# Kernel tuning notes

Hardware: AMD Instinct MI355X
Metric: run time of the kernel (lower is better)

The kernel has to match this reference:

```python
import jax, jax.numpy as jnp
import numpy as np

B, T, C, H = 65536, 100, 7, 2  # batch, timesteps, covariates, lstm hidden


def setup_inputs() -> dict:
    key = jax.random.key(0)
    ks = iter(jax.random.split(key, 32))
    def rn(shape, s=0.1):
        return jax.random.normal(next(ks), shape, dtype=jnp.float32) * s
    inp = {"x": jax.random.normal(next(ks), (B, T, C), dtype=jnp.float32)}
    for l, din in ((0, C), (1, 2 * H)):
        for suf in ("", "r"):
            inp[f"w_ih_l{l}{suf}"] = rn((4 * H, din))
            inp[f"w_hh_l{l}{suf}"] = rn((4 * H, H))
            inp[f"b_ih_l{l}{suf}"] = rn((4 * H,))
            inp[f"b_hh_l{l}{suf}"] = rn((4 * H,))
    inp["fc1_w"] = rn((64, 4 * T))
    inp["fc1_b"] = rn((64,))
    inp["fc2_w"] = rn((20, 64))
    inp["fc2_b"] = rn((20,))
    return inp


def _lstm_dir(xw, w_hh, b_hh, reverse):
    # xw: [T, B, 4H] precomputed input projection (x @ W_ih.T + b_ih)
    if reverse:
        xw = xw[::-1]
    h0 = jnp.zeros((xw.shape[1], H), xw.dtype)
    c0 = jnp.zeros((xw.shape[1], H), xw.dtype)

    def step(carry, gx):
        h, c = carry
        g = gx + h @ w_hh.T + b_hh            # [B, 4H]
        i, f, gg, o = jnp.split(g, 4, axis=-1)  # torch gate order i,f,g,o
        c = jax.nn.sigmoid(f) * c + jax.nn.sigmoid(i) * jnp.tanh(gg)
        h = jax.nn.sigmoid(o) * jnp.tanh(c)
        return (h, c), h

    _, hs = jax.lax.scan(step, (h0, c0), xw)
    if reverse:
        hs = hs[::-1]
    return hs  # [T, B, H]


def _bilstm_layer(x_tbf, w_ih_f, w_hh_f, b_ih_f, b_hh_f,
                  w_ih_b, w_hh_b, b_ih_b, b_hh_b):
    xw_f = jnp.einsum('tbc,gc->tbg', x_tbf, w_ih_f) + b_ih_f
    xw_b = jnp.einsum('tbc,gc->tbg', x_tbf, w_ih_b) + b_ih_b
    hf = _lstm_dir(xw_f, w_hh_f, b_hh_f, False)
    hb = _lstm_dir(xw_b, w_hh_b, b_hh_b, True)
    return jnp.concatenate([hf, hb], axis=-1)  # [T, B, 2H]


def reference(x,
              w_ih_l0, w_hh_l0, b_ih_l0, b_hh_l0,
              w_ih_l0r, w_hh_l0r, b_ih_l0r, b_hh_l0r,
              w_ih_l1, w_hh_l1, b_ih_l1, b_hh_l1,
              w_ih_l1r, w_hh_l1r, b_ih_l1r, b_hh_l1r,
              fc1_w, fc1_b, fc2_w, fc2_b):
    xt = jnp.transpose(x.reshape(-1, T, C), (1, 0, 2))  # [T, B, C] time-major
    h1 = _bilstm_layer(xt, w_ih_l0, w_hh_l0, b_ih_l0, b_hh_l0,
                       w_ih_l0r, w_hh_l0r, b_ih_l0r, b_hh_l0r)
    h2 = _bilstm_layer(h1, w_ih_l1, w_hh_l1, b_ih_l1, b_hh_l1,
                       w_ih_l1r, w_hh_l1r, b_ih_l1r, b_hh_l1r)
    out = jnp.transpose(h2, (1, 0, 2)).reshape(-1, 4 * T)  # flatten [B, 4T]
    out = jax.nn.relu(out)                  # relu BEFORE fc1, as in original
    out = jax.nn.relu(out @ fc1_w.T + fc1_b)
    return out @ fc2_w.T + fc2_b            # [B, 20]
```

## Files before the change

kernel.cpp:

```cpp
#include <hip/hip_runtime.h>

#define Bn 65536
#define Tn 100
#define Cn 7

__device__ __forceinline__ float fast_rcp(float x) { return __builtin_amdgcn_rcpf(x); }
__device__ __forceinline__ float sig_f(float x) { return fast_rcp(1.f + __expf(-x)); }
__device__ __forceinline__ float tanh_f(float x) { return 1.f - 2.f * fast_rcp(__expf(2.f * x) + 1.f); }
__device__ __forceinline__ float rdlane(float v, int l) {
    return __int_as_float(__builtin_amdgcn_readlane(__float_as_int(v), l));
}

typedef const __attribute__((address_space(1))) void* gp_t;
typedef __attribute__((address_space(3))) void* sp_t;
__device__ __forceinline__ void async_copy_dw(const float* g, float* l) {
    __builtin_amdgcn_global_load_lds((gp_t)g, (sp_t)l, 4, 0, 0);
}

__global__ void fc1t_kernel(const float* __restrict__ fc1_w, float* __restrict__ fc1_wt) {
    int idx = blockIdx.x * 256 + threadIdx.x;
    if (idx < 400 * 64) {
        int col = idx >> 6;
        int k = idx & 63;
        fc1_wt[idx] = fc1_w[k * 400 + col];
    }
}

__global__ __launch_bounds__(256) void l0_kernel(
    const float* __restrict__ x,
    const float* __restrict__ wih_f, const float* __restrict__ whh_f,
    const float* __restrict__ bih_f, const float* __restrict__ bhh_f,
    const float* __restrict__ wih_r, const float* __restrict__ whh_r,
    const float* __restrict__ bih_r, const float* __restrict__ bhh_r,
    float2* __restrict__ h1f2)
{
    __shared__ float xs[2][2][4480];

    const int tid  = threadIdx.x;
    const int rev  = tid >> 7;
    const int s    = tid & 127;
    const int b    = blockIdx.x * 128 + s;
    const int w    = tid >> 6;
    const int lane = tid & 63;
    const int sdir = w >> 1;
    const int half = w & 1;

    const float* wih = rev ? wih_r : wih_f;
    const float* whh = rev ? whh_r : whh_f;
    const float* bih = rev ? bih_r : bih_f;
    const float* bhh = rev ? bhh_r : bhh_f;

    float wi[56], wh[16], bias[8];
#pragma unroll
    for (int k = 0; k < 56; ++k) wi[k] = wih[k];
#pragma unroll
    for (int k = 0; k < 16; ++k) wh[k] = whh[k];
#pragma unroll
    for (int k = 0; k < 8; ++k) bias[k] = bih[k] + bhh[k];

    const int e  = (lane >= 35) ? 1 : 0;
    const int r0 = lane - 35 * e;
    const int s0 = half * 64 + e;
    const float* xsamp = x + (size_t)(blockIdx.x * 128 + s0) * 700;

    auto stage = [&](int ch, int p) {
        const int off = sdir ? (665 - 35 * ch) : (35 * ch);
        const float* g = xsamp + off + r0;
        float* l = &xs[p][sdir][half * 2240 + lane];
        int r = r0;
#pragma unroll
        for (int i = 0; i < 35; ++i) {
            async_copy_dw(g, l);
            l += 64;
            const int c = (r >= 6) ? 1 : 0;
            g += c ? 1394 : 729;
            r += c ? -6 : 29;
        }
    };

    float h0 = 0.f, h1v = 0.f, c0 = 0.f, c1 = 0.f;

    stage(0, 0);
#pragma unroll 1
    for (int ch = 0; ch < 20; ++ch) {
        __builtin_amdgcn_s_waitcnt(0);
        __syncthreads();
        if (ch < 19) stage(ch + 1, (ch + 1) & 1);

        const int t0 = rev ? (95 - 5 * ch) : (5 * ch);
        const float* xbuf = &xs[ch & 1][rev][0];
#pragma unroll 1
        for (int tt = 0; tt < 5; ++tt) {
            const int rr = rev ? (4 - tt) : tt;
            const int t  = t0 + rr;
            const float* xrow = xbuf + s * 35 + rr * 7;

            float g[8];
#pragma unroll
            for (int k = 0; k < 8; ++k) g[k] = bias[k];
#pragma unroll
            for (int c = 0; c < 7; ++c) {
                const float xv = xrow[c];
#pragma unroll
                for (int k = 0; k < 8; ++k) g[k] = fmaf(wi[k * 7 + c], xv, g[k]);
            }
#pragma unroll
            for (int k = 0; k < 8; ++k)
                g[k] = fmaf(wh[k * 2], h0, fmaf(wh[k * 2 + 1], h1v, g[k]));

            const float i0 = sig_f(g[0]), i1 = sig_f(g[1]);
            const float f0 = sig_f(g[2]), f1 = sig_f(g[3]);
            const float q0 = tanh_f(g[4]), q1 = tanh_f(g[5]);
            const float o0 = sig_f(g[6]), o1 = sig_f(g[7]);
            c0 = fmaf(f0, c0, i0 * q0);
            c1 = fmaf(f1, c1, i1 * q1);
            h0  = o0 * tanh_f(c0);
            h1v = o1 * tanh_f(c1);

            h1f2[((size_t)t * 2 + rev) * Bn + b] = make_float2(h0, h1v);
        }
    }
}

__global__ __launch_bounds__(256) void l1fc_kernel(
    const float2* __restrict__ hin,
    const float* __restrict__ wih_f, const float* __restrict__ whh_f,
    const float* __restrict__ bih_f, const float* __restrict__ bhh_f,
    const float* __restrict__ wih_r, const float* __restrict__ whh_r,
    const float* __restrict__ bih_r, const float* __restrict__ bhh_r,
    const float* __restrict__ fc1_wt,
    const float* __restrict__ fc1_b,
    const float* __restrict__ fc2_w,
    const float* __restrict__ fc2_b,
    float* __restrict__ out)
{
    __shared__ float ebuf[128 * 65];

    const int tid  = threadIdx.x;
    const int w    = tid >> 6;
    const int lane = tid & 63;
    const int d    = w >> 1;
    const int half = w & 1;
    const int sm   = half * 64 + lane;
    const size_t b = (size_t)blockIdx.x * 128 + sm;

    const float* wih = d ? wih_r : wih_f;
    const float* whh = d ? whh_r : whh_f;
    const float* bih = d ? bih_r : bih_f;
    const float* bhh = d ? bhh_r : bhh_f;

    float wi[32], wh[16], bias[8];
#pragma unroll
    for (int k = 0; k < 32; ++k) wi[k] = wih[k];
#pragma unroll
    for (int k = 0; k < 16; ++k) wh[k] = whh[k];
#pragma unroll
    for (int k = 0; k < 8; ++k) bias[k] = bih[k] + bhh[k];

    const float b1 = fc1_b[lane];

    float acc[64];
#pragma unroll
    for (int k = 0; k < 64; ++k) acc[k] = 0.f;

    auto tstep = [&](int st) { return d ? 99 - st : st; };
    auto hload = [&](int t, float2& uF, float2& uR) {
        uF = hin[((size_t)t * 2) * Bn + b];
        uR = hin[((size_t)t * 2 + 1) * Bn + b];
    };
    auto wrow = [&](int t) { return fc1_wt + ((size_t)t * 4 + 2 * d) * 64 + lane; };

    float2 aF, aR, p1F, p1R, p2F, p2R;
    hload(tstep(0), aF, aR);
    hload(tstep(1), p1F, p1R);
    hload(tstep(2), p2F, p2R);
    float wt0, wt1;
    { const float* wr = wrow(tstep(0)); wt0 = wr[0]; wt1 = wr[64]; }

    float h0 = 0.f, h1v = 0.f, c0 = 0.f, c1 = 0.f;

#pragma unroll 1
    for (int st = 0; st < 100; ++st) {
        const int sp = (st + 3 <= 99) ? st + 3 : 99;
        float2 nF, nR;
        hload(tstep(sp), nF, nR);
        const float* wr = wrow(tstep((st + 1 <= 99) ? st + 1 : 99));
        const float nw0 = wr[0], nw1 = wr[64];

        float g[8];
#pragma unroll
        for (int k = 0; k < 8; ++k) {
            g[k] = bias[k];
            g[k] = fmaf(wi[k * 4 + 0], aF.x, g[k]);
            g[k] = fmaf(wi[k * 4 + 1], aF.y, g[k]);
            g[k] = fmaf(wi[k * 4 + 2], aR.x, g[k]);
            g[k] = fmaf(wi[k * 4 + 3], aR.y, g[k]);
            g[k] = fmaf(wh[k * 2], h0, fmaf(wh[k * 2 + 1], h1v, g[k]));
        }
        const float i0 = sig_f(g[0]), i1 = sig_f(g[1]);
        const float f0 = sig_f(g[2]), f1 = sig_f(g[3]);
        const float q0 = tanh_f(g[4]), q1 = tanh_f(g[5]);
        const float o0 = sig_f(g[6]), o1 = sig_f(g[7]);
        c0 = fmaf(f0, c0, i0 * q0);
        c1 = fmaf(f1, c1, i1 * q1);
        h0  = o0 * tanh_f(c0);
        h1v = o1 * tanh_f(c1);

        const float v0 = fmaxf(h0, 0.f);
        const float v1 = fmaxf(h1v, 0.f);
#pragma unroll
        for (int j = 0; j < 64; ++j)
            acc[j] = fmaf(wt0, rdlane(v0, j), fmaf(wt1, rdlane(v1, j), acc[j]));

        aF = p1F; aR = p1R; p1F = p2F; p1R = p2R; p2F = nF; p2R = nR;
        wt0 = nw0; wt1 = nw1;
    }

    if (d) {
#pragma unroll
        for (int j = 0; j < 64; ++j) ebuf[(half * 64 + j) * 65 + lane] = acc[j];
    }
    __syncthreads();
    if (!d) {
#pragma unroll
        for (int j = 0; j < 64; ++j) {
            const int row = half * 64 + j;
            const float z = acc[j] + ebuf[row * 65 + lane] + b1;
            ebuf[row * 65 + lane] = fmaxf(z, 0.f);
        }
    }
    __syncthreads();

    const int sm2 = tid & 127;
    const int og  = (tid >> 7) * 10;
    float z[64];
#pragma unroll
    for (int k = 0; k < 64; ++k) z[k] = ebuf[sm2 * 65 + k];
    float y[10];
#pragma unroll
    for (int o = 0; o < 10; ++o) {
        float r2 = fc2_b[og + o];
#pragma unroll
        for (int k = 0; k < 64; ++k) r2 = fmaf(fc2_w[(og + o) * 64 + k], z[k], r2);
        y[o] = r2;
    }
    __syncthreads();
#pragma unroll
    for (int o = 0; o < 10; ++o) ebuf[sm2 * 20 + og + o] = y[o];
    __syncthreads();
    for (int f = tid; f < 2560; f += 256)
        out[(size_t)blockIdx.x * 2560 + f] = ebuf[f];
}

extern "C" void kernel_launch(void* const* d_in, const int* in_sizes, int n_in,
                              void* d_out, int out_size, void* d_ws, size_t ws_size,
                              hipStream_t stream) {
    const float* x = (const float*)d_in[0];
    const float* w_ih_l0  = (const float*)d_in[1];
    const float* w_hh_l0  = (const float*)d_in[2];
    const float* b_ih_l0  = (const float*)d_in[3];
    const float* b_hh_l0  = (const float*)d_in[4];
    const float* w_ih_l0r = (const float*)d_in[5];
    const float* w_hh_l0r = (const float*)d_in[6];
    const float* b_ih_l0r = (const float*)d_in[7];
    const float* b_hh_l0r = (const float*)d_in[8];
    const float* w_ih_l1  = (const float*)d_in[9];
    const float* w_hh_l1  = (const float*)d_in[10];
    const float* b_ih_l1  = (const float*)d_in[11];
    const float* b_hh_l1  = (const float*)d_in[12];
    const float* w_ih_l1r = (const float*)d_in[13];
    const float* w_hh_l1r = (const float*)d_in[14];
    const float* b_ih_l1r = (const float*)d_in[15];
    const float* b_hh_l1r = (const float*)d_in[16];
    const float* fc1_w = (const float*)d_in[17];
    const float* fc1_b = (const float*)d_in[18];
    const float* fc2_w = (const float*)d_in[19];
    const float* fc2_b = (const float*)d_in[20];

    float2* h1f2  = (float2*)d_ws;
    float* fc1_wt = (float*)((char*)d_ws + (size_t)Tn * 4 * Bn * sizeof(float));

    fc1t_kernel<<<100, 256, 0, stream>>>(fc1_w, fc1_wt);
    l0_kernel<<<512, 256, 0, stream>>>(x,
        w_ih_l0, w_hh_l0, b_ih_l0, b_hh_l0,
        w_ih_l0r, w_hh_l0r, b_ih_l0r, b_hh_l0r, h1f2);
    l1fc_kernel<<<512, 256, 0, stream>>>(h1f2,
        w_ih_l1, w_hh_l1, b_ih_l1, b_hh_l1,
        w_ih_l1r, w_hh_l1r, b_ih_l1r, b_hh_l1r,
        fc1_wt, fc1_b, fc2_w, fc2_b, (float*)d_out);
}
```

Before: 490.4 us.

## Compute fc1 with bf16 MFMA over staged LSTM outputs instead of readlane FMAs

Replaces the per-timestep 64-wide readlane/FMA accumulation of fc1 with staging relu'd layer-1 hidden states as packed bf16 in LDS, in chunks of 25 timesteps. Each chunk then runs 16x16x32 bf16 MFMA tiles against a pre-arranged bf16 copy of fc1 weights built by a new prep kernel. This removes the large scalar-broadcast FMA loop from the recurrence and frees the 64-float accumulator registers. In exchange it adds per-chunk block syncs and LDS traffic, and the bf16 rounding of activations and weights lowers precision.

```diff
diff --git a/kernel.cpp b/kernel.cpp
--- a/kernel.cpp
+++ b/kernel.cpp
@@ -4,11 +4,15 @@
 #define Tn 100
 #define Cn 7
 
+typedef short short8 __attribute__((ext_vector_type(8)));
+typedef float float4v __attribute__((ext_vector_type(4)));
+
 __device__ __forceinline__ float fast_rcp(float x) { return __builtin_amdgcn_rcpf(x); }
 __device__ __forceinline__ float sig_f(float x) { return fast_rcp(1.f + __expf(-x)); }
 __device__ __forceinline__ float tanh_f(float x) { return 1.f - 2.f * fast_rcp(__expf(2.f * x) + 1.f); }
-__device__ __forceinline__ float rdlane(float v, int l) {
-    return __int_as_float(__builtin_amdgcn_readlane(__float_as_int(v), l));
+__device__ __forceinline__ unsigned bf16rne(float x) {
+    unsigned u = __float_as_uint(x);
+    return (u + 0x7fffu + ((u >> 16) & 1u)) >> 16;
 }
 
 typedef const __attribute__((address_space(1))) void* gp_t;
@@ -17,13 +21,13 @@
     __builtin_amdgcn_global_load_lds((gp_t)g, (sp_t)l, 4, 0, 0);
 }
 
-__global__ void fc1t_kernel(const float* __restrict__ fc1_w, float* __restrict__ fc1_wt) {
+__global__ void w2prep_kernel(const float* __restrict__ fc1_w, unsigned short* __restrict__ w2g) {
     int idx = blockIdx.x * 256 + threadIdx.x;
-    if (idx < 400 * 64) {
-        int col = idx >> 6;
-        int k = idx & 63;
-        fc1_wt[idx] = fc1_w[k * 400 + col];
-    }
+    int w = idx >> 13, d = (idx >> 12) & 1, n = (idx >> 6) & 63, kk = idx & 63;
+    int tt = kk >> 1, i = kk & 1;
+    int t = d ? (99 - 25 * w - tt) : (25 * w + tt);
+    float v = (kk < 50) ? fc1_w[n * 400 + 4 * t + 2 * d + i] : 0.f;
+    w2g[idx] = (unsigned short)bf16rne(v);
 }
 
 __global__ __launch_bounds__(256) void l0_kernel(
@@ -128,19 +132,20 @@
     const float* __restrict__ bih_f, const float* __restrict__ bhh_f,
     const float* __restrict__ wih_r, const float* __restrict__ whh_r,
     const float* __restrict__ bih_r, const float* __restrict__ bhh_r,
-    const float* __restrict__ fc1_wt,
+    const float4* __restrict__ w2g,
     const float* __restrict__ fc1_b,
     const float* __restrict__ fc2_w,
     const float* __restrict__ fc2_b,
     float* __restrict__ out)
 {
-    __shared__ float ebuf[128 * 65];
+    __shared__ unsigned a2[2 * 128 * 36];
+    __shared__ unsigned w2[2 * 64 * 36];
 
     const int tid  = threadIdx.x;
-    const int w    = tid >> 6;
+    const int ww   = tid >> 6;
     const int lane = tid & 63;
-    const int d    = w >> 1;
-    const int half = w & 1;
+    const int d    = ww >> 1;
+    const int half = ww & 1;
     const int sm   = half * 64 + lane;
     const size_t b = (size_t)blockIdx.x * 128 + sm;
 
@@ -157,85 +162,124 @@
 #pragma unroll
     for (int k = 0; k < 8; ++k) bias[k] = bih[k] + bhh[k];
 
-    const float b1 = fc1_b[lane];
-
-    float acc[64];
-#pragma unroll
-    for (int k = 0; k < 64; ++k) acc[k] = 0.f;
+    float4v acc[2][4];
+#pragma unroll
+    for (int mt = 0; mt < 2; ++mt)
+#pragma unroll
+        for (int nt = 0; nt < 4; ++nt) acc[mt][nt] = (float4v){0.f, 0.f, 0.f, 0.f};
+
+    for (int i2 = tid; i2 < 2 * 128 * 36; i2 += 256) a2[i2] = 0u;
+    __syncthreads();
 
     auto tstep = [&](int st) { return d ? 99 - st : st; };
     auto hload = [&](int t, float2& uF, float2& uR) {
         uF = hin[((size_t)t * 2) * Bn + b];
         uR = hin[((size_t)t * 2 + 1) * Bn + b];
     };
-    auto wrow = [&](int t) { return fc1_wt + ((size_t)t * 4 + 2 * d) * 64 + lane; };
 
     float2 aF, aR, p1F, p1R, p2F, p2R;
     hload(tstep(0), aF, aR);
     hload(tstep(1), p1F, p1R);
     hload(tstep(2), p2F, p2R);
-    float wt0, wt1;
-    { const float* wr = wrow(tstep(0)); wt0 = wr[0]; wt1 = wr[64]; }
 
     float h0 = 0.f, h1v = 0.f, c0 = 0.f, c1 = 0.f;
+    const int cbase = tid * 4;
 
 #pragma unroll 1
-    for (int st = 0; st < 100; ++st) {
-        const int sp = (st + 3 <= 99) ? st + 3 : 99;
-        float2 nF, nR;
-        hload(tstep(sp), nF, nR);
-        const float* wr = wrow(tstep((st + 1 <= 99) ? st + 1 : 99));
-        const float nw0 = wr[0], nw1 = wr[64];
-
-        float g[8];
-#pragma unroll
-        for (int k = 0; k < 8; ++k) {
-            g[k] = bias[k];
-            g[k] = fmaf(wi[k * 4 + 0], aF.x, g[k]);
-            g[k] = fmaf(wi[k * 4 + 1], aF.y, g[k]);
-            g[k] = fmaf(wi[k * 4 + 2], aR.x, g[k]);
-            g[k] = fmaf(wi[k * 4 + 3], aR.y, g[k]);
-            g[k] = fmaf(wh[k * 2], h0, fmaf(wh[k * 2 + 1], h1v, g[k]));
-        }
-        const float i0 = sig_f(g[0]), i1 = sig_f(g[1]);
-        const float f0 = sig_f(g[2]), f1 = sig_f(g[3]);
-        const float q0 = tanh_f(g[4]), q1 = tanh_f(g[5]);
-        const float o0 = sig_f(g[6]), o1 = sig_f(g[7]);
-        c0 = fmaf(f0, c0, i0 * q0);
-        c1 = fmaf(f1, c1, i1 * q1);
-        h0  = o0 * tanh_f(c0);
-        h1v = o1 * tanh_f(c1);
-
-        const float v0 = fmaxf(h0, 0.f);
-        const float v1 = fmaxf(h1v, 0.f);
-#pragma unroll
-        for (int j = 0; j < 64; ++j)
-            acc[j] = fmaf(wt0, rdlane(v0, j), fmaf(wt1, rdlane(v1, j), acc[j]));
-
-        aF = p1F; aR = p1R; p1F = p2F; p1R = p2R; p2F = nF; p2R = nR;
-        wt0 = nw0; wt1 = nw1;
+    for (int w = 0; w < 4; ++w) {
+        float4 wl[4];
+#pragma unroll
+        for (int j = 0; j < 4; ++j) wl[j] = w2g[w * 1024 + cbase + j];
+
+#pragma unroll 1
+        for (int tt = 0; tt < 25; ++tt) {
+            const int st = 25 * w + tt;
+            const int sp = (st + 3 <= 99) ? st + 3 : 99;
+            float2 nF, nR;
+            hload(tstep(sp), nF, nR);
+
+            float g[8];
+#pragma unroll
+            for (int k = 0; k < 8; ++k) {
+                g[k] = bias[k];
+                g[k] = fmaf(wi[k * 4 + 0], aF.x, g[k]);
+                g[k] = fmaf(wi[k * 4 + 1], aF.y, g[k]);
+                g[k] = fmaf(wi[k * 4 + 2], aR.x, g[k]);
+                g[k] = fmaf(wi[k * 4 + 3], aR.y, g[k]);
+                g[k] = fmaf(wh[k * 2], h0, fmaf(wh[k * 2 + 1], h1v, g[k]));
+            }
+            const float i0 = sig_f(g[0]), i1 = sig_f(g[1]);
+            const float f0 = sig_f(g[2]), f1 = sig_f(g[3]);
+            const float q0 = tanh_f(g[4]), q1 = tanh_f(g[5]);
+            const float o0 = sig_f(g[6]), o1 = sig_f(g[7]);
+            c0 = fmaf(f0, c0, i0 * q0);
+            c1 = fmaf(f1, c1, i1 * q1);
+            h0  = o0 * tanh_f(c0);
+            h1v = o1 * tanh_f(c1);
+
+            const unsigned vpk = bf16rne(fmaxf(h0, 0.f)) | (bf16rne(fmaxf(h1v, 0.f)) << 16);
+            a2[d * 4608 + sm * 36 + tt] = vpk;
+
+            aF = p1F; aR = p1R; p1F = p2F; p1R = p2R; p2F = nF; p2R = nR;
+        }
+
+#pragma unroll
+        for (int j = 0; j < 4; ++j) {
+            const int c = cbase + j;
+            const int dst = (((c >> 9) << 6) + ((c >> 3) & 63)) * 36 + (c & 7) * 4;
+            *(float4*)(&w2[dst]) = wl[j];
+        }
+        __syncthreads();
+
+        {
+            const int q = lane >> 4, l16 = lane & 15;
+#pragma unroll
+            for (int dd = 0; dd < 2; ++dd) {
+#pragma unroll
+                for (int kt = 0; kt < 2; ++kt) {
+                    short8 av[2], bv[4];
+#pragma unroll
+                    for (int mt = 0; mt < 2; ++mt) {
+                        const int srow = ww * 32 + mt * 16 + l16;
+                        av[mt] = *(const short8*)&a2[dd * 4608 + srow * 36 + kt * 16 + q * 4];
+                    }
+#pragma unroll
+                    for (int nt = 0; nt < 4; ++nt)
+                        bv[nt] = *(const short8*)&w2[(dd * 64 + nt * 16 + l16) * 36 + kt * 16 + q * 4];
+#pragma unroll
+                    for (int mt = 0; mt < 2; ++mt)
+#pragma unroll
+                        for (int nt = 0; nt < 4; ++nt)
+                            acc[mt][nt] = __builtin_amdgcn_mfma_f32_16x16x32_bf16(
+                                av[mt], bv[nt], acc[mt][nt], 0, 0, 0);
+                }
+            }
+        }
+        __syncthreads();
     }
 
-    if (d) {
-#pragma unroll
-        for (int j = 0; j < 64; ++j) ebuf[(half * 64 + j) * 65 + lane] = acc[j];
+    {
+        const int q = lane >> 4, l16 = lane & 15;
+        float* eb = (float*)a2;
+#pragma unroll
+        for (int mt = 0; mt < 2; ++mt)
+#pragma unroll
+            for (int nt = 0; nt < 4; ++nt)
+#pragma unroll
+                for (int r = 0; r < 4; ++r) {
+                    const int sl = ww * 32 + mt * 16 + q * 4 + r;
+                    const int cl = nt * 16 + l16;
+                    eb[sl * 65 + cl] = acc[mt][nt][r];
+                }
     }
     __syncthreads();
-    if (!d) {
-#pragma unroll
-        for (int j = 0; j < 64; ++j) {
-            const int row = half * 64 + j;
-            const float z = acc[j] + ebuf[row * 65 + lane] + b1;
-            ebuf[row * 65 + lane] = fmaxf(z, 0.f);
-        }
-    }
-    __syncthreads();
-
+
+    const float* eb = (const float*)a2;
     const int sm2 = tid & 127;
     const int og  = (tid >> 7) * 10;
     float z[64];
 #pragma unroll
-    for (int k = 0; k < 64; ++k) z[k] = ebuf[sm2 * 65 + k];
+    for (int k = 0; k < 64; ++k) z[k] = fmaxf(eb[sm2 * 65 + k] + fc1_b[k], 0.f);
     float y[10];
 #pragma unroll
     for (int o = 0; o < 10; ++o) {
@@ -245,11 +289,12 @@
         y[o] = r2;
     }
     __syncthreads();
-#pragma unroll
-    for (int o = 0; o < 10; ++o) ebuf[sm2 * 20 + og + o] = y[o];
+    float* ebw = (float*)a2;
+#pragma unroll
+    for (int o = 0; o < 10; ++o) ebw[sm2 * 20 + og + o] = y[o];
     __syncthreads();
     for (int f = tid; f < 2560; f += 256)
-        out[(size_t)blockIdx.x * 2560 + f] = ebuf[f];
+        out[(size_t)blockIdx.x * 2560 + f] = ebw[f];
 }
 
 extern "C" void kernel_launch(void* const* d_in, const int* in_sizes, int n_in,
@@ -277,15 +322,15 @@
     const float* fc2_w = (const float*)d_in[19];
     const float* fc2_b = (const float*)d_in[20];
 
-    float2* h1f2  = (float2*)d_ws;
-    float* fc1_wt = (float*)((char*)d_ws + (size_t)Tn * 4 * Bn * sizeof(float));
-
-    fc1t_kernel<<<100, 256, 0, stream>>>(fc1_w, fc1_wt);
+    float2* h1f2 = (float2*)d_ws;
+    unsigned short* w2g = (unsigned short*)((char*)d_ws + (size_t)Tn * 4 * Bn * sizeof(float));
+
+    w2prep_kernel<<<128, 256, 0, stream>>>(fc1_w, w2g);
     l0_kernel<<<512, 256, 0, stream>>>(x,
         w_ih_l0, w_hh_l0, b_ih_l0, b_hh_l0,
         w_ih_l0r, w_hh_l0r, b_ih_l0r, b_hh_l0r, h1f2);
     l1fc_kernel<<<512, 256, 0, stream>>>(h1f2,
         w_ih_l1, w_hh_l1, b_ih_l1, b_hh_l1,
         w_ih_l1r, w_hh_l1r, b_ih_l1r, b_hh_l1r,
-        fc1_wt, fc1_b, fc2_w, fc2_b, (float*)d_out);
-}
+        (const float4*)w2g, fc1_b, fc2_w, fc2_b, (float*)d_out);
+}
```

Measured after the change: 468.7 us. 1.05x faster.
